# Performance work log

Measured on AMD Instinct MI355X. Metric: run time of the kernel, lower is better.

Reference implementation:

```python
import jax, jax.numpy as jnp
import numpy as np

LEAK = 0.3
SPECTRAL_RADIUS = 0.9
SPARSITY = 0.9
B, T, IN, H, R, OUT = 64, 512, 256, 512, 512, 10


def _linear_params(key, fan_in, fan_out):
    kw, kb = jax.random.split(key)
    s = 1.0 / np.sqrt(fan_in)
    W = jax.random.uniform(kw, (fan_in, fan_out), jnp.float32, -s, s)
    b = jax.random.uniform(kb, (fan_out,), jnp.float32, -s, s)
    return W, b


def _reservoir(seed, size):
    rng = np.random.default_rng(seed)
    W = rng.standard_normal((size, size)).astype(np.float32)
    mask = rng.random((size, size)) > SPARSITY
    W = W * mask
    rad = np.abs(np.linalg.eigvals(W)).max().real
    return jnp.asarray(W * (SPECTRAL_RADIUS / rad), dtype=jnp.float32)


def setup_inputs() -> dict:
    key = jax.random.key(0)
    keys = jax.random.split(key, 32)
    inp = {}
    inp['x'] = jax.random.normal(keys[0], (B, T, IN), dtype=jnp.float32)
    ki = 1
    for li, lin in [(0, IN), (1, H)]:
        p = f'L{li}_'
        inp[p + 'Win'] = 1.0 * jax.random.normal(keys[ki], (lin, R), dtype=jnp.float32); ki += 1
        inp[p + 'Wres'] = _reservoir(100 + li, R)
        inp[p + 'Wz'], inp[p + 'bz'] = _linear_params(keys[ki], lin + H, H); ki += 1
        inp[p + 'Wr'], inp[p + 'br'] = _linear_params(keys[ki], lin + H, H); ki += 1
        inp[p + 'Wc'], inp[p + 'bc'] = _linear_params(keys[ki], lin + H, H); ki += 1
        inp[p + 'Wg'], inp[p + 'bg'] = _linear_params(keys[ki], lin + H + R, H); ki += 1
        inp[p + 'Wp'], inp[p + 'bp'] = _linear_params(keys[ki], R, H); ki += 1
    inp['Wo1'], inp['bo1'] = _linear_params(keys[ki], H, H); ki += 1
    inp['Wo2'], inp['bo2'] = _linear_params(keys[ki], H, OUT); ki += 1
    return inp


def _run_layer(x, Win, Wres, Wz, bz, Wr, br, Wc, bc, Wg, bg, Wp, bp):
    # x: (B, T, lin) -> outputs (B, T, H)
    b = x.shape[0]
    h0 = jnp.zeros((b, H), x.dtype)
    r0 = jnp.zeros((b, R), x.dtype)

    def step(carry, x_t):
        r, h = carry
        r = (1.0 - LEAK) * r + LEAK * jnp.tanh(x_t @ Win + r @ Wres)
        comb = jnp.concatenate([x_t, h], axis=1)
        z = jax.nn.sigmoid(comb @ Wz + bz)
        reset = jax.nn.sigmoid(comb @ Wr + br)
        cand = jnp.tanh(jnp.concatenate([x_t, reset * h], axis=1) @ Wc + bc)
        h_gru = (1.0 - z) * h + z * cand
        g = jax.nn.sigmoid(jnp.concatenate([x_t, h_gru, r], axis=1) @ Wg + bg)
        h_new = (1.0 - g) * h_gru + g * jnp.tanh(r @ Wp + bp)
        return (r, h_new), h_new

    _, ys = jax.lax.scan(step, (r0, h0), jnp.swapaxes(x, 0, 1))
    return jnp.swapaxes(ys, 0, 1)  # (B, T, H)


def reference(x,
              L0_Win, L0_Wres, L0_Wz, L0_bz, L0_Wr, L0_br, L0_Wc, L0_bc, L0_Wg, L0_bg, L0_Wp, L0_bp,
              L1_Win, L1_Wres, L1_Wz, L1_bz, L1_Wr, L1_br, L1_Wc, L1_bc, L1_Wg, L1_bg, L1_Wp, L1_bp,
              Wo1, bo1, Wo2, bo2):
    h = _run_layer(x, L0_Win, L0_Wres, L0_Wz, L0_bz, L0_Wr, L0_br, L0_Wc, L0_bc, L0_Wg, L0_bg, L0_Wp, L0_bp)
    # dropout p=0.0 (eval) -> identity
    h = _run_layer(h, L1_Win, L1_Wres, L1_Wz, L1_bz, L1_Wr, L1_br, L1_Wc, L1_bc, L1_Wg, L1_bg, L1_Wp, L1_bp)
    last = h[:, -1, :]
    out = jax.nn.relu(last @ Wo1 + bo1) @ Wo2 + bo2
    return out
```

## Files before the change

### kernel.cpp

```cpp
#include <hip/hip_runtime.h>
#include <math.h>

static constexpr int Tt   = 512;
static constexpr int INF  = 256;
static constexpr int Hf   = 512;
static constexpr int OUTF = 10;
static constexpr int NBLK = 256;
static constexpr int NTHR = 1024;
static constexpr int SGLOB = Tt + 2;
static constexpr unsigned SMEM_BYTES = 98304 + 49152 + 4096;

__device__ __forceinline__ float sigmoidf_(float x) {
    return 1.0f / (1.0f + __expf(-x));
}
__device__ __forceinline__ float tanhf_(float x) {
    float e = __expf(-2.0f * fabsf(x));
    float r = (1.0f - e) / (1.0f + e);
    return copysignf(r, x);
}

__device__ __forceinline__ float ldc(const float* p) {
    return __hip_atomic_load(const_cast<float*>(p), __ATOMIC_RELAXED, __HIP_MEMORY_SCOPE_AGENT);
}
__device__ __forceinline__ void stc(float* p, float v) {
    __hip_atomic_store(p, v, __ATOMIC_RELAXED, __HIP_MEMORY_SCOPE_AGENT);
}

__device__ __forceinline__ void arrive_(unsigned* flags, unsigned gen) {
    asm volatile("s_waitcnt vmcnt(0)" ::: "memory");
    __syncthreads();
    if (threadIdx.x == 0)
        __hip_atomic_store(&flags[blockIdx.x], gen, __ATOMIC_RELAXED, __HIP_MEMORY_SCOPE_AGENT);
}
__device__ __forceinline__ void wait_(unsigned* flags, unsigned gen) {
    if (threadIdx.x < NBLK) {
        unsigned* f = &flags[threadIdx.x];
        while (__hip_atomic_load(f, __ATOMIC_RELAXED, __HIP_MEMORY_SCOPE_AGENT) < gen)
            __builtin_amdgcn_s_sleep(1);
    }
    __syncthreads();
}

__global__ __launch_bounds__(256) void transpose_x_k(const float* __restrict__ x,
                                                     float* __restrict__ xT) {
    __shared__ float tile[64][65];
    int t  = blockIdx.x;
    int k0 = blockIdx.y * 64;
    int tid = threadIdx.x;
#pragma unroll
    for (int i = 0; i < 16; ++i) {
        int idx = i * 256 + tid;
        int bb = idx >> 6, kk = idx & 63;
        tile[bb][kk] = x[(size_t)bb * Tt * INF + (size_t)t * INF + k0 + kk];
    }
    __syncthreads();
#pragma unroll
    for (int i = 0; i < 16; ++i) {
        int idx = i * 256 + tid;
        int kk = idx >> 6, bb = idx & 63;
        xT[(size_t)t * INF * 64 + (size_t)(k0 + kk) * 64 + bb] = tile[bb][kk];
    }
}

#define FMA4(a, w, v) { (a).x = fmaf((w).x, (v), (a).x); (a).y = fmaf((w).y, (v), (a).y); \
                        (a).z = fmaf((w).z, (v), (a).z); (a).w = fmaf((w).w, (v), (a).w); }

template<bool SC>
__device__ __forceinline__ float ldx(const float* p) { return SC ? ldc(p) : *p; }

template<int L16, bool SC>
__device__ __forceinline__ void xw2(const float* xs, int lane, int wv,
                                    const float4* w0, const float4* w1,
                                    float4& a0, float4& a1) {
    const int kb = wv * L16;
    float xv[L16];
#pragma unroll
    for (int i = 0; i < L16; ++i) xv[i] = ldx<SC>(xs + (size_t)(kb + i) * 64 + lane);
#pragma unroll
    for (int i = 0; i < L16; ++i) {
        float4 w = w0[kb + i]; FMA4(a0, w, xv[i]);
        w = w1[kb + i];        FMA4(a1, w, xv[i]);
    }
}
template<int L16, bool SC>
__device__ __forceinline__ void xw3(const float* xs, int lane, int wv,
                                    const float4* w0, const float4* w1, const float4* w2,
                                    float4& a0, float4& a1, float4& a2) {
    const int kb = wv * L16;
    float xv[L16];
#pragma unroll
    for (int i = 0; i < L16; ++i) xv[i] = ldx<SC>(xs + (size_t)(kb + i) * 64 + lane);
#pragma unroll
    for (int i = 0; i < L16; ++i) {
        float4 w = w0[kb + i]; FMA4(a0, w, xv[i]);
        w = w1[kb + i];        FMA4(a1, w, xv[i]);
        w = w2[kb + i];        FMA4(a2, w, xv[i]);
    }
}

template<int LIN, bool XSC, bool WY>
__device__ __forceinline__ void run_layer(
    const float* __restrict__ xsrc, float* y0,
    float* r0, float* r1, float* h0, float* h1, float* rhB, float* hgB,
    const float* __restrict__ Win, const float* __restrict__ Wres,
    const float* __restrict__ Wz, const float* __restrict__ bz,
    const float* __restrict__ Wr, const float* __restrict__ br,
    const float* __restrict__ Wc, const float* __restrict__ bc,
    const float* __restrict__ Wg, const float* __restrict__ bg,
    const float* __restrict__ Wp, const float* __restrict__ bp,
    unsigned* flags, int c0, int tshift)
{
    constexpr int L16 = LIN / 16;
    extern __shared__ char smem[];
    float4* wRESx = (float4*)smem;
    float4* wRESs = wRESx + LIN;
    float4* wZx   = wRESs + 512;
    float4* wZs   = wZx + LIN;
    float4* wRx   = wZs + 512;
    float4* wRs   = wRx + LIN;
    float4* wCx   = wRs + 512;
    float4* wCs   = wCx + LIN;
    float4* wGx   = wCs + 512;
    float4* wGh   = wGx + LIN;
    float4* wGr   = wGh + 512;
    float4* wP    = wGr + 512;
    float* pb  = (float*)(smem + (size_t)(5 * LIN + 3584) * 16);
    float* lz  = pb + 12288;
    float* lp  = lz + 256;
    float* lgg = lp + 256;
    float* lhg = lgg + 256;

    const int tid  = threadIdx.x;
    const int lane = tid & 63;
    const int wv   = tid >> 6;

    for (int k = tid; k < LIN; k += NTHR) {
        wRESx[k] = *(const float4*)&Win[(size_t)k * 512 + c0];
        wZx[k]   = *(const float4*)&Wz[(size_t)k * 512 + c0];
        wRx[k]   = *(const float4*)&Wr[(size_t)k * 512 + c0];
        wCx[k]   = *(const float4*)&Wc[(size_t)k * 512 + c0];
        wGx[k]   = *(const float4*)&Wg[(size_t)k * 512 + c0];
    }
    for (int k = tid; k < 512; k += NTHR) {
        wRESs[k] = *(const float4*)&Wres[(size_t)k * 512 + c0];
        wZs[k]   = *(const float4*)&Wz[(size_t)(LIN + k) * 512 + c0];
        wRs[k]   = *(const float4*)&Wr[(size_t)(LIN + k) * 512 + c0];
        wCs[k]   = *(const float4*)&Wc[(size_t)(LIN + k) * 512 + c0];
        wGh[k]   = *(const float4*)&Wg[(size_t)(LIN + k) * 512 + c0];
        wGr[k]   = *(const float4*)&Wg[(size_t)(LIN + 512 + k) * 512 + c0];
        wP[k]    = *(const float4*)&Wp[(size_t)k * 512 + c0];
    }
    __syncthreads();

    const int m    = tid >> 8;
    const int rrem = tid & 255;
    const int cdx  = rrem >> 6;
    const int rbb  = rrem & 63;
    const int cab  = c0 + cdx;
    const int gi   = cab * 64 + rbb;
    float bzr = 0, brr = 0, bcr = 0, bpr = 0, bgr = 0;
    if (tid < 768) {
        bzr = bz[cab]; brr = br[cab]; bcr = bc[cab]; bpr = bp[cab]; bgr = bg[cab];
    }

#define PB_WRITE(mm, v) { \
    pb[(((mm)*4+0)*16+wv)*64+lane] = (v).x; \
    pb[(((mm)*4+1)*16+wv)*64+lane] = (v).y; \
    pb[(((mm)*4+2)*16+wv)*64+lane] = (v).z; \
    pb[(((mm)*4+3)*16+wv)*64+lane] = (v).w; }

    unsigned gen = 0;
    const float4 z4 = {0.f, 0.f, 0.f, 0.f};
    float4 cRES = z4, cZ = z4, cR = z4, cX = z4, cG = z4;
    const int ks = wv * 32;

    if (tshift == 0)
        xw3<L16, XSC>(xsrc, lane, wv, wRESx, wZx, wRx, cRES, cZ, cR);

    for (int s = 0; s < SGLOB; ++s) {
        const int t = s - tshift;
        const bool act = (t >= 0) && (t < Tt);
        const bool wn  = (t + 1 >= 0) && (t + 1 < Tt);
        float* rc = (t & 1) ? r1 : r0;
        float* rn = (t & 1) ? r0 : r1;
        float* hc = (t & 1) ? h1 : h0;
        float* hn = (t & 1) ? h0 : h1;
        const float* xs_t = xsrc + (size_t)(act ? t : 0) * LIN * 64;
        const float* xs_n = xsrc + (size_t)(wn ? (t + 1) : 0) * LIN * 64;

        wait_(flags, gen);
        if (act) {
            float ownR = 0.f, ownH = 0.f;
            if (tid < 768) { if (m == 0) ownR = ldc(rc + gi); else if (m == 2) ownH = ldc(hc + gi); }
            float rv[32], hv[32];
#pragma unroll
            for (int i = 0; i < 32; ++i) rv[i] = ldc(rc + (size_t)(ks + i) * 64 + lane);
#pragma unroll
            for (int i = 0; i < 32; ++i) hv[i] = ldc(hc + (size_t)(ks + i) * 64 + lane);
            float4 aRES = cRES, aZ = cZ, aR = cR;
#pragma unroll
            for (int i = 0; i < 32; ++i) { float4 w = wRESs[ks + i]; FMA4(aRES, w, rv[i]); }
#pragma unroll
            for (int i = 0; i < 32; ++i) {
                float4 w = wZs[ks + i]; FMA4(aZ, w, hv[i]);
                w = wRs[ks + i];        FMA4(aR, w, hv[i]);
            }
            PB_WRITE(0, aRES); PB_WRITE(1, aZ); PB_WRITE(2, aR);
            __syncthreads();
            if (tid < 768) {
                float sa = 0.f;
#pragma unroll
                for (int w = 0; w < 16; ++w) sa += pb[((m * 4 + cdx) * 16 + w) * 64 + rbb];
                if (m == 0)      stc(rn + gi, 0.7f * ownR + 0.3f * tanhf_(sa));
                else if (m == 1) lz[rrem] = sigmoidf_(sa + bzr);
                else             stc(rhB + gi, sigmoidf_(sa + brr) * ownH);
            }
        }
        arrive_(flags, ++gen);
        if (act) { cX = z4; cG = z4; xw2<L16, XSC>(xs_t, lane, wv, wCx, wGx, cX, cG); }
        wait_(flags, gen);

        if (act) {
            float ownH = 0.f;
            if (tid < 768 && m == 0) ownH = ldc(hc + gi);
            float rnv[32], rhv[32];
#pragma unroll
            for (int i = 0; i < 32; ++i) rnv[i] = ldc(rn + (size_t)(ks + i) * 64 + lane);
#pragma unroll
            for (int i = 0; i < 32; ++i) rhv[i] = ldc(rhB + (size_t)(ks + i) * 64 + lane);
            float4 aC = cX, aP = z4, aG = cG;
#pragma unroll
            for (int i = 0; i < 32; ++i) {
                float4 w = wP[ks + i];  FMA4(aP, w, rnv[i]);
                w = wGr[ks + i];        FMA4(aG, w, rnv[i]);
            }
#pragma unroll
            for (int i = 0; i < 32; ++i) { float4 w = wCs[ks + i]; FMA4(aC, w, rhv[i]); }
            PB_WRITE(0, aC); PB_WRITE(1, aP); PB_WRITE(2, aG);
            __syncthreads();
            if (tid < 768) {
                float sa = 0.f;
#pragma unroll
                for (int w = 0; w < 16; ++w) sa += pb[((m * 4 + cdx) * 16 + w) * 64 + rbb];
                if (m == 0) {
                    float cand = tanhf_(sa + bcr);
                    float zv = lz[rrem];
                    float hg = (1.f - zv) * ownH + zv * cand;
                    stc(hgB + gi, hg);
                    lhg[rrem] = hg;
                } else if (m == 1) {
                    lp[rrem] = tanhf_(sa + bpr);
                } else {
                    lgg[rrem] = sa;
                }
            }
        }
        arrive_(flags, ++gen);
        if (wn) { cRES = z4; cZ = z4; cR = z4;
                  xw3<L16, XSC>(xs_n, lane, wv, wRESx, wZx, wRx, cRES, cZ, cR); }
        wait_(flags, gen);

        if (act) {
            float hgv[32];
#pragma unroll
            for (int i = 0; i < 32; ++i) hgv[i] = ldc(hgB + (size_t)(ks + i) * 64 + lane);
            float4 aGh = z4;
#pragma unroll
            for (int i = 0; i < 32; ++i) { float4 w = wGh[ks + i]; FMA4(aGh, w, hgv[i]); }
            PB_WRITE(0, aGh);
            __syncthreads();
            if (tid < 256) {
                float sa = 0.f;
#pragma unroll
                for (int w = 0; w < 16; ++w) sa += pb[((cdx) * 16 + w) * 64 + rbb];
                float g = sigmoidf_(sa + lgg[rrem] + bgr);
                float hnv = (1.f - g) * lhg[rrem] + g * lp[rrem];
                stc(hn + gi, hnv);
                if (WY) stc(y0 + (size_t)t * (Hf * 64) + gi, hnv);
            }
        }
        arrive_(flags, ++gen);
    }
#undef PB_WRITE
}

struct KParams {
    const float* xT0;
    float* y0;
    const float *Win0,*Wres0,*Wz0,*bz0,*Wr0,*br0,*Wc0,*bc0,*Wg0,*bg0,*Wp0,*bp0;
    const float *Win1,*Wres1,*Wz1,*bz1,*Wr1,*br1,*Wc1,*bc1,*Wg1,*bg1,*Wp1,*bp1;
    float *r00,*r01,*h00,*h01,*rh0,*hg0;
    float *r10,*r11,*h10,*h11,*rh1,*hg1;
    unsigned* flags;
};

__global__ __launch_bounds__(NTHR) void esn_dual_k(KParams P)
{
    const int bid = blockIdx.x;
    const int c0  = (bid & 127) * 4;
    if (bid < 128) {
        run_layer<INF, false, true>(P.xT0, P.y0,
            P.r00, P.r01, P.h00, P.h01, P.rh0, P.hg0,
            P.Win0, P.Wres0, P.Wz0, P.bz0, P.Wr0, P.br0,
            P.Wc0, P.bc0, P.Wg0, P.bg0, P.Wp0, P.bp0,
            P.flags, c0, 0);
    } else {
        run_layer<Hf, true, false>(P.y0, nullptr,
            P.r10, P.r11, P.h10, P.h11, P.rh1, P.hg1,
            P.Win1, P.Wres1, P.Wz1, P.bz1, P.Wr1, P.br1,
            P.Wc1, P.bc1, P.Wg1, P.bg1, P.Wp1, P.bp1,
            P.flags, c0, 2);
    }
}

__global__ __launch_bounds__(256) void head1_k(const float* __restrict__ hlast,
                                               const float* __restrict__ Wo1,
                                               const float* __restrict__ bo1,
                                               float* __restrict__ hidT) {
    int tid = threadIdx.x;
    int b = tid & 63, jg = tid >> 6;
    int j0 = blockIdx.x * 16 + jg * 4;
    float acc[4] = {0.f, 0.f, 0.f, 0.f};
    const float* ap = hlast + b;
    const float* wp = Wo1 + j0;
#pragma unroll 4
    for (int k = 0; k < Hf; ++k) {
        float xv = ap[k * 64];
        const float4 w = *reinterpret_cast<const float4*>(wp + k * 512);
        acc[0] = fmaf(w.x, xv, acc[0]);
        acc[1] = fmaf(w.y, xv, acc[1]);
        acc[2] = fmaf(w.z, xv, acc[2]);
        acc[3] = fmaf(w.w, xv, acc[3]);
    }
#pragma unroll
    for (int jj = 0; jj < 4; ++jj) {
        int j = j0 + jj;
        hidT[j * 64 + b] = fmaxf(acc[jj] + bo1[j], 0.f);
    }
}

__global__ __launch_bounds__(640) void head2_k(const float* __restrict__ hidT,
                                               const float* __restrict__ Wo2,
                                               const float* __restrict__ bo2,
                                               float* __restrict__ out) {
    int tid = threadIdx.x;
    if (tid >= 64 * OUTF) return;
    int b = tid / OUTF, o = tid % OUTF;
    float acc = 0.f;
    for (int k = 0; k < Hf; ++k)
        acc = fmaf(hidT[k * 64 + b], Wo2[k * OUTF + o], acc);
    out[tid] = acc + bo2[o];
}

extern "C" void kernel_launch(void* const* d_in, const int* in_sizes, int n_in,
                              void* d_out, int out_size, void* d_ws, size_t ws_size,
                              hipStream_t stream) {
    const float* x = (const float*)d_in[0];
    const float* W[2][12];
    int idx = 1;
    for (int li = 0; li < 2; ++li)
        for (int j = 0; j < 12; ++j) W[li][j] = (const float*)d_in[idx++];
    const float* Wo1 = (const float*)d_in[idx++];
    const float* bo1 = (const float*)d_in[idx++];
    const float* Wo2 = (const float*)d_in[idx++];
    const float* bo2 = (const float*)d_in[idx++];

    char* ws = (char*)d_ws;
    size_t off = 0;
    auto walloc = [&](size_t bytes) -> float* {
        float* p = (float*)(ws + off);
        off += (bytes + 255) & ~(size_t)255;
        return p;
    };
    const size_t STATE = (size_t)Hf * 64 * sizeof(float);
    float* xT0 = walloc((size_t)Tt * INF * 64 * sizeof(float));
    float* y0  = walloc((size_t)Tt * Hf * 64 * sizeof(float));
    KParams P;
    P.xT0 = xT0; P.y0 = y0;
    P.Win0 = W[0][0]; P.Wres0 = W[0][1]; P.Wz0 = W[0][2]; P.bz0 = W[0][3];
    P.Wr0 = W[0][4]; P.br0 = W[0][5]; P.Wc0 = W[0][6]; P.bc0 = W[0][7];
    P.Wg0 = W[0][8]; P.bg0 = W[0][9]; P.Wp0 = W[0][10]; P.bp0 = W[0][11];
    P.Win1 = W[1][0]; P.Wres1 = W[1][1]; P.Wz1 = W[1][2]; P.bz1 = W[1][3];
    P.Wr1 = W[1][4]; P.br1 = W[1][5]; P.Wc1 = W[1][6]; P.bc1 = W[1][7];
    P.Wg1 = W[1][8]; P.bg1 = W[1][9]; P.Wp1 = W[1][10]; P.bp1 = W[1][11];
    P.r00 = walloc(STATE); P.r01 = walloc(STATE);
    P.h00 = walloc(STATE); P.h01 = walloc(STATE);
    P.rh0 = walloc(STATE); P.hg0 = walloc(STATE);
    P.r10 = walloc(STATE); P.r11 = walloc(STATE);
    P.h10 = walloc(STATE); P.h11 = walloc(STATE);
    P.rh1 = walloc(STATE); P.hg1 = walloc(STATE);
    float* hidT = walloc(STATE);
    P.flags = (unsigned*)walloc(NBLK * sizeof(unsigned));
    (void)ws_size;

    hipFuncSetAttribute((const void*)esn_dual_k,
                        hipFuncAttributeMaxDynamicSharedMemorySize, SMEM_BYTES);

    transpose_x_k<<<dim3(Tt, INF / 64), 256, 0, stream>>>(x, xT0);

    hipMemsetAsync(P.flags, 0, NBLK * sizeof(unsigned), stream);
    hipMemsetAsync(P.r00, 0, STATE, stream);
    hipMemsetAsync(P.h00, 0, STATE, stream);
    hipMemsetAsync(P.r10, 0, STATE, stream);
    hipMemsetAsync(P.h10, 0, STATE, stream);

    esn_dual_k<<<NBLK, NTHR, SMEM_BYTES, stream>>>(P);

    head1_k<<<dim3(32, 1), 256, 0, stream>>>(P.h10, Wo1, bo1, hidT);
    head2_k<<<dim3(1, 1), 640, 0, stream>>>(hidT, Wo2, bo2, (float*)d_out);
}
```

Measured before the change: 37.52 ms.

## Switch state buffers to batch-major layout with vectorized coherent 16-byte loads

Changes the shared recurrent state and per-timestep input buffers from feature-major [k][batch] to batch-major [batch][k]. Each lane can then fetch its 32 contiguous features with eight dwordx4 loads carrying the sc1 cache bit, instead of 32 scalar atomic loads. This is meant to cut the number of memory instructions on the latency-bound cross-block exchange path that runs every step. In exchange, lanes now access strided rows (512 floats apart), which breaks coalescing across the wavefront, and the inline asm waits on vmcnt(0) right after issuing, so the loads cannot overlap with other work.

```diff
diff --git a/kernel.cpp b/kernel.cpp
--- a/kernel.cpp
+++ b/kernel.cpp
@@ -26,6 +26,22 @@
     __hip_atomic_store(p, v, __ATOMIC_RELAXED, __HIP_MEMORY_SCOPE_AGENT);
 }
 
+__device__ __forceinline__ void ldc4x8(const float* p, float4* o) {
+    asm volatile(
+        "global_load_dwordx4 %0, %8, off sc1\n\t"
+        "global_load_dwordx4 %1, %8, off offset:16 sc1\n\t"
+        "global_load_dwordx4 %2, %8, off offset:32 sc1\n\t"
+        "global_load_dwordx4 %3, %8, off offset:48 sc1\n\t"
+        "global_load_dwordx4 %4, %8, off offset:64 sc1\n\t"
+        "global_load_dwordx4 %5, %8, off offset:80 sc1\n\t"
+        "global_load_dwordx4 %6, %8, off offset:96 sc1\n\t"
+        "global_load_dwordx4 %7, %8, off offset:112 sc1\n\t"
+        "s_waitcnt vmcnt(0)"
+        : "=&v"(o[0]), "=&v"(o[1]), "=&v"(o[2]), "=&v"(o[3]),
+          "=&v"(o[4]), "=&v"(o[5]), "=&v"(o[6]), "=&v"(o[7])
+        : "v"(p) : "memory");
+}
+
 __device__ __forceinline__ void arrive_(unsigned* flags, unsigned gen) {
     asm volatile("s_waitcnt vmcnt(0)" ::: "memory");
     __syncthreads();
@@ -43,58 +59,57 @@
 
 __global__ __launch_bounds__(256) void transpose_x_k(const float* __restrict__ x,
                                                      float* __restrict__ xT) {
-    __shared__ float tile[64][65];
-    int t  = blockIdx.x;
-    int k0 = blockIdx.y * 64;
-    int tid = threadIdx.x;
-#pragma unroll
-    for (int i = 0; i < 16; ++i) {
-        int idx = i * 256 + tid;
-        int bb = idx >> 6, kk = idx & 63;
-        tile[bb][kk] = x[(size_t)bb * Tt * INF + (size_t)t * INF + k0 + kk];
-    }
-    __syncthreads();
-#pragma unroll
-    for (int i = 0; i < 16; ++i) {
-        int idx = i * 256 + tid;
-        int kk = idx >> 6, bb = idx & 63;
-        xT[(size_t)t * INF * 64 + (size_t)(k0 + kk) * 64 + bb] = tile[bb][kk];
-    }
+    int t = blockIdx.x;
+    int b = threadIdx.x >> 2;
+    int q = threadIdx.x & 3;
+    const float4* src = (const float4*)(x + ((size_t)b * Tt + t) * INF + q * 64);
+    float4* dst = (float4*)(xT + ((size_t)t * 64 + b) * INF + q * 64);
+#pragma unroll
+    for (int i = 0; i < 16; ++i) dst[i] = src[i];
 }
 
 #define FMA4(a, w, v) { (a).x = fmaf((w).x, (v), (a).x); (a).y = fmaf((w).y, (v), (a).y); \
                         (a).z = fmaf((w).z, (v), (a).z); (a).w = fmaf((w).w, (v), (a).w); }
 
-template<bool SC>
-__device__ __forceinline__ float ldx(const float* p) { return SC ? ldc(p) : *p; }
-
-template<int L16, bool SC>
+template<int LIN, int L16, bool SC>
+__device__ __forceinline__ void xload(const float* xs, int lane, int kb, float4* o) {
+    if constexpr (SC) {
+        static_assert(L16 == 32, "scoped path is 8x16B");
+        ldc4x8(xs + (size_t)lane * LIN + kb, o);
+    } else {
+        const float4* p = (const float4*)(xs + (size_t)lane * LIN + kb);
+#pragma unroll
+        for (int i = 0; i < L16 / 4; ++i) o[i] = p[i];
+    }
+}
+
+template<int LIN, int L16, bool SC>
 __device__ __forceinline__ void xw2(const float* xs, int lane, int wv,
                                     const float4* w0, const float4* w1,
                                     float4& a0, float4& a1) {
     const int kb = wv * L16;
-    float xv[L16];
-#pragma unroll
-    for (int i = 0; i < L16; ++i) xv[i] = ldx<SC>(xs + (size_t)(kb + i) * 64 + lane);
+    float4 xv4[L16 / 4];
+    xload<LIN, L16, SC>(xs, lane, kb, xv4);
+    const float* xf = (const float*)xv4;
 #pragma unroll
     for (int i = 0; i < L16; ++i) {
-        float4 w = w0[kb + i]; FMA4(a0, w, xv[i]);
-        w = w1[kb + i];        FMA4(a1, w, xv[i]);
-    }
-}
-template<int L16, bool SC>
+        float4 w = w0[kb + i]; FMA4(a0, w, xf[i]);
+        w = w1[kb + i];        FMA4(a1, w, xf[i]);
+    }
+}
+template<int LIN, int L16, bool SC>
 __device__ __forceinline__ void xw3(const float* xs, int lane, int wv,
                                     const float4* w0, const float4* w1, const float4* w2,
                                     float4& a0, float4& a1, float4& a2) {
     const int kb = wv * L16;
-    float xv[L16];
-#pragma unroll
-    for (int i = 0; i < L16; ++i) xv[i] = ldx<SC>(xs + (size_t)(kb + i) * 64 + lane);
+    float4 xv4[L16 / 4];
+    xload<LIN, L16, SC>(xs, lane, kb, xv4);
+    const float* xf = (const float*)xv4;
 #pragma unroll
     for (int i = 0; i < L16; ++i) {
-        float4 w = w0[kb + i]; FMA4(a0, w, xv[i]);
-        w = w1[kb + i];        FMA4(a1, w, xv[i]);
-        w = w2[kb + i];        FMA4(a2, w, xv[i]);
+        float4 w = w0[kb + i]; FMA4(a0, w, xf[i]);
+        w = w1[kb + i];        FMA4(a1, w, xf[i]);
+        w = w2[kb + i];        FMA4(a2, w, xf[i]);
     }
 }
 
@@ -157,7 +172,7 @@
     const int cdx  = rrem >> 6;
     const int rbb  = rrem & 63;
     const int cab  = c0 + cdx;
-    const int gi   = cab * 64 + rbb;
+    const int gi   = rbb * 512 + cab;
     float bzr = 0, brr = 0, bcr = 0, bpr = 0, bgr = 0;
     if (tid < 768) {
         bzr = bz[cab]; brr = br[cab]; bcr = bc[cab]; bpr = bp[cab]; bgr = bg[cab];
@@ -175,7 +190,7 @@
     const int ks = wv * 32;
 
     if (tshift == 0)
-        xw3<L16, XSC>(xsrc, lane, wv, wRESx, wZx, wRx, cRES, cZ, cR);
+        xw3<LIN, L16, XSC>(xsrc, lane, wv, wRESx, wZx, wRx, cRES, cZ, cR);
 
     for (int s = 0; s < SGLOB; ++s) {
         const int t = s - tshift;
@@ -192,18 +207,18 @@
         if (act) {
             float ownR = 0.f, ownH = 0.f;
             if (tid < 768) { if (m == 0) ownR = ldc(rc + gi); else if (m == 2) ownH = ldc(hc + gi); }
-            float rv[32], hv[32];
-#pragma unroll
-            for (int i = 0; i < 32; ++i) rv[i] = ldc(rc + (size_t)(ks + i) * 64 + lane);
-#pragma unroll
-            for (int i = 0; i < 32; ++i) hv[i] = ldc(hc + (size_t)(ks + i) * 64 + lane);
-            float4 aRES = cRES, aZ = cZ, aR = cR;
-#pragma unroll
-            for (int i = 0; i < 32; ++i) { float4 w = wRESs[ks + i]; FMA4(aRES, w, rv[i]); }
+            float4 sv4[8];
+            ldc4x8(rc + (size_t)lane * 512 + ks, sv4);
+            const float* svf = (const float*)sv4;
+            float4 aRES = cRES;
+#pragma unroll
+            for (int i = 0; i < 32; ++i) { float4 w = wRESs[ks + i]; FMA4(aRES, w, svf[i]); }
+            ldc4x8(hc + (size_t)lane * 512 + ks, sv4);
+            float4 aZ = cZ, aR = cR;
 #pragma unroll
             for (int i = 0; i < 32; ++i) {
-                float4 w = wZs[ks + i]; FMA4(aZ, w, hv[i]);
-                w = wRs[ks + i];        FMA4(aR, w, hv[i]);
+                float4 w = wZs[ks + i]; FMA4(aZ, w, svf[i]);
+                w = wRs[ks + i];        FMA4(aR, w, svf[i]);
             }
             PB_WRITE(0, aRES); PB_WRITE(1, aZ); PB_WRITE(2, aR);
             __syncthreads();
@@ -217,25 +232,25 @@
             }
         }
         arrive_(flags, ++gen);
-        if (act) { cX = z4; cG = z4; xw2<L16, XSC>(xs_t, lane, wv, wCx, wGx, cX, cG); }
+        if (act) { cX = z4; cG = z4; xw2<LIN, L16, XSC>(xs_t, lane, wv, wCx, wGx, cX, cG); }
         wait_(flags, gen);
 
         if (act) {
             float ownH = 0.f;
             if (tid < 768 && m == 0) ownH = ldc(hc + gi);
-            float rnv[32], rhv[32];
-#pragma unroll
-            for (int i = 0; i < 32; ++i) rnv[i] = ldc(rn + (size_t)(ks + i) * 64 + lane);
-#pragma unroll
-            for (int i = 0; i < 32; ++i) rhv[i] = ldc(rhB + (size_t)(ks + i) * 64 + lane);
-            float4 aC = cX, aP = z4, aG = cG;
+            float4 sv4[8];
+            ldc4x8(rn + (size_t)lane * 512 + ks, sv4);
+            const float* svf = (const float*)sv4;
+            float4 aP = z4, aG = cG;
 #pragma unroll
             for (int i = 0; i < 32; ++i) {
-                float4 w = wP[ks + i];  FMA4(aP, w, rnv[i]);
-                w = wGr[ks + i];        FMA4(aG, w, rnv[i]);
+                float4 w = wP[ks + i];  FMA4(aP, w, svf[i]);
+                w = wGr[ks + i];        FMA4(aG, w, svf[i]);
             }
-#pragma unroll
-            for (int i = 0; i < 32; ++i) { float4 w = wCs[ks + i]; FMA4(aC, w, rhv[i]); }
+            ldc4x8(rhB + (size_t)lane * 512 + ks, sv4);
+            float4 aC = cX;
+#pragma unroll
+            for (int i = 0; i < 32; ++i) { float4 w = wCs[ks + i]; FMA4(aC, w, svf[i]); }
             PB_WRITE(0, aC); PB_WRITE(1, aP); PB_WRITE(2, aG);
             __syncthreads();
             if (tid < 768) {
@@ -257,16 +272,16 @@
         }
         arrive_(flags, ++gen);
         if (wn) { cRES = z4; cZ = z4; cR = z4;
-                  xw3<L16, XSC>(xs_n, lane, wv, wRESx, wZx, wRx, cRES, cZ, cR); }
+                  xw3<LIN, L16, XSC>(xs_n, lane, wv, wRESx, wZx, wRx, cRES, cZ, cR); }
         wait_(flags, gen);
 
         if (act) {
-            float hgv[32];
-#pragma unroll
-            for (int i = 0; i < 32; ++i) hgv[i] = ldc(hgB + (size_t)(ks + i) * 64 + lane);
+            float4 sv4[8];
+            ldc4x8(hgB + (size_t)lane * 512 + ks, sv4);
+            const float* svf = (const float*)sv4;
             float4 aGh = z4;
 #pragma unroll
-            for (int i = 0; i < 32; ++i) { float4 w = wGh[ks + i]; FMA4(aGh, w, hgv[i]); }
+            for (int i = 0; i < 32; ++i) { float4 w = wGh[ks + i]; FMA4(aGh, w, svf[i]); }
             PB_WRITE(0, aGh);
             __syncthreads();
             if (tid < 256) {
@@ -321,11 +336,11 @@
     int b = tid & 63, jg = tid >> 6;
     int j0 = blockIdx.x * 16 + jg * 4;
     float acc[4] = {0.f, 0.f, 0.f, 0.f};
-    const float* ap = hlast + b;
+    const float* ap = hlast + (size_t)b * 512;
     const float* wp = Wo1 + j0;
 #pragma unroll 4
     for (int k = 0; k < Hf; ++k) {
-        float xv = ap[k * 64];
+        float xv = ap[k];
         const float4 w = *reinterpret_cast<const float4*>(wp + k * 512);
         acc[0] = fmaf(w.x, xv, acc[0]);
         acc[1] = fmaf(w.y, xv, acc[1]);
@@ -396,7 +411,7 @@
     hipFuncSetAttribute((const void*)esn_dual_k,
                         hipFuncAttributeMaxDynamicSharedMemorySize, SMEM_BYTES);
 
-    transpose_x_k<<<dim3(Tt, INF / 64), 256, 0, stream>>>(x, xT0);
+    transpose_x_k<<<dim3(Tt), 256, 0, stream>>>(x, xT0);
 
     hipMemsetAsync(P.flags, 0, NBLK * sizeof(unsigned), stream);
     hipMemsetAsync(P.r00, 0, STATE, stream);
```

Result: slower. 131.4 ms (+250.2%).
